# Kernel tuning notes

Measured on AMD Instinct MI355X. Metric: run time of the kernel, lower is better.

## Reference

```python
import jax, jax.numpy as jnp
import numpy as np
from jax import lax

K = 5
SCALE = 100.0
IN_CHN = 128
OUT_CHN = 128
KS = 3
STRIDE = 1
PAD = 1
N_W = OUT_CHN * IN_CHN * KS * KS


def setup_inputs() -> dict:
    key = jax.random.key(0)
    k1, k2, k3, k4, k5 = jax.random.split(key, 5)
    x = jax.random.normal(k1, (32, IN_CHN, 56, 56), dtype=jnp.float32)
    Alpha = jax.random.uniform(k2, (OUT_CHN, 1, 1), dtype=jnp.float32)
    # xavier-normal-ish init for M, Z
    M = jax.random.normal(k3, (OUT_CHN, IN_CHN, KS, KS), dtype=jnp.float32) * 0.05
    Z = jax.random.normal(k4, (K, OUT_CHN, IN_CHN, KS, KS), dtype=jnp.float32) * 0.05
    # rv ~ N(0, 1/sqrt(scale)) of shape (1, K); sample is all-zeros so the random branch is taken
    rv = jax.random.normal(k5, (1, K), dtype=jnp.float32) / np.float32(np.sqrt(SCALE))
    return {"x": x, "Alpha": Alpha, "M": M, "Z": Z, "rv": rv}


def reference(x, Alpha, M, Z, rv):
    # --- SDP weight synthesis (normalization is done under no_grad in torch) ---
    m = M.reshape(N_W)                # (N,)
    z = Z.reshape(K, N_W)             # (K, N)
    A = m * m + jnp.sum(z * z, axis=0) / SCALE
    inv = lax.rsqrt(A)
    m_n = m * inv
    z_n = z * inv
    w = (rv @ z_n + m_n).reshape(OUT_CHN, IN_CHN, KS, KS)  # (O,I,k,k)
    # --- sign binarization of weights and activations (ReCU) ---
    bw = jnp.sign(w)
    ba = jnp.sign(x)
    # --- conv2d, NCHW/OIHW ---
    out = lax.conv_general_dilated(
        ba, bw,
        window_strides=(STRIDE, STRIDE),
        padding=[(PAD, PAD), (PAD, PAD)],
        dimension_numbers=("NCHW", "OIHW", "NCHW"),
    )
    out = out * Alpha  # Alpha (O,1,1) broadcasts over (B,O,H,W)
    return out
```

## Files before the change

### kernel.cpp

```cpp
#include <hip/hip_runtime.h>
#include <stdint.h>

typedef unsigned int u32;
typedef unsigned long long u64;

#define HW      3136
#define PADW    58
#define PADHW   3364

#define WB_OFF   0
#define BF_OFF   18432
#define N2A_OFF  23040
#define AB_OFF   23552

#define NB_W     128
#define NB_A     392
#define NB_R     29

__global__ __launch_bounds__(256) void k_prep(
    const float* __restrict__ x, const float* __restrict__ Alpha,
    const float* __restrict__ M, const float* __restrict__ Z,
    const float* __restrict__ rv, char* __restrict__ ws)
{
  int t = threadIdx.x;
  if (blockIdx.x < NB_W) {
    u32*   wb  = (u32*)(ws + WB_OFF);
    float* Bf  = (float*)(ws + BF_OFF);
    float* n2a = (float*)(ws + N2A_OFF);
    __shared__ float sw[1152];
    __shared__ u32 sbits[36];
    __shared__ int spc[9];
    int o = blockIdx.x;
    float r0 = rv[0], r1 = rv[1], r2 = rv[2], r3 = rv[3], r4 = rv[4];
    const float4* M4 = (const float4*)M;
    const float4* Z4 = (const float4*)Z;
    float4* sw4 = (float4*)sw;

    for (int j = t; j < 288; j += 256) {
      float4 a = M4[o * 288 + j];
      float4 z;
      z = Z4[0 * 36864 + o * 288 + j];
      a.x = fmaf(r0, z.x, a.x); a.y = fmaf(r0, z.y, a.y);
      a.z = fmaf(r0, z.z, a.z); a.w = fmaf(r0, z.w, a.w);
      z = Z4[1 * 36864 + o * 288 + j];
      a.x = fmaf(r1, z.x, a.x); a.y = fmaf(r1, z.y, a.y);
      a.z = fmaf(r1, z.z, a.z); a.w = fmaf(r1, z.w, a.w);
      z = Z4[2 * 36864 + o * 288 + j];
      a.x = fmaf(r2, z.x, a.x); a.y = fmaf(r2, z.y, a.y);
      a.z = fmaf(r2, z.z, a.z); a.w = fmaf(r2, z.w, a.w);
      z = Z4[3 * 36864 + o * 288 + j];
      a.x = fmaf(r3, z.x, a.x); a.y = fmaf(r3, z.y, a.y);
      a.z = fmaf(r3, z.z, a.z); a.w = fmaf(r3, z.w, a.w);
      z = Z4[4 * 36864 + o * 288 + j];
      a.x = fmaf(r4, z.x, a.x); a.y = fmaf(r4, z.y, a.y);
      a.z = fmaf(r4, z.z, a.z); a.w = fmaf(r4, z.w, a.w);
      sw4[j] = a;
    }
    __syncthreads();

    if (t < 36) {
      int tap = t >> 2;
      int wd  = t & 3;
      u32 bits = 0;
#pragma unroll
      for (int c = 0; c < 32; ++c) {
        float v = sw[(wd * 32 + c) * 9 + tap];
        bits |= (v > 0.0f ? 1u : 0u) << c;
      }
      wb[(o * 9 + tap) * 4 + wd] = bits;
      sbits[t] = bits;
    }
    __syncthreads();
    if (t < 9)
      spc[t] = __popc(sbits[4 * t]) + __popc(sbits[4 * t + 1])
             + __popc(sbits[4 * t + 2]) + __popc(sbits[4 * t + 3]);
    __syncthreads();
    if (t < 9) {
      int ht = t / 3, wt = t - ht * 3;
      int corr = 0;
#pragma unroll
      for (int tap = 0; tap < 9; ++tap) {
        int dh = tap / 3, dw = tap - dh * 3;
        int inv = ((ht == 0) & (dh == 0)) | ((ht == 2) & (dh == 2)) |
                  ((wt == 0) & (dw == 0)) | ((wt == 2) & (dw == 2));
        if (inv) corr += 128 - 2 * spc[tap];
      }
      Bf[t * 128 + o] = (float)(1152 - corr) * Alpha[o];
    }
    if (t == 0) n2a[o] = -2.0f * Alpha[o];
  } else if (blockIdx.x < NB_W + NB_A) {
    u32* abw = (u32*)(ws + AB_OFF);
    int idx = (blockIdx.x - NB_W) * 256 + t;
    int bg  = idx / 784;
    int q   = idx - bg * 784;
    int b   = bg >> 2;
    int g   = bg & 3;
    int h   = q / 14;
    int w0  = (q - h * 14) * 4;

    const float4* X4 = (const float4*)x
        + ((size_t)b * 128 + g * 32) * (HW / 4) + q;
    u32 m0 = 0, m1 = 0, m2 = 0, m3 = 0;
#pragma unroll
    for (int c = 0; c < 32; ++c) {
      float4 f = X4[(size_t)c * (HW / 4)];
      m0 |= (f.x > 0.0f ? 1u : 0u) << c;
      m1 |= (f.y > 0.0f ? 1u : 0u) << c;
      m2 |= (f.z > 0.0f ? 1u : 0u) << c;
      m3 |= (f.w > 0.0f ? 1u : 0u) << c;
    }
    size_t base = ((size_t)b * PADHW + (h + 1) * PADW + (w0 + 1)) * 4 + g;
    abw[base]      = m0;
    abw[base + 4]  = m1;
    abw[base + 8]  = m2;
    abw[base + 12] = m3;
  } else {
    uint4* ab4 = (uint4*)(ws + AB_OFF);
    int e = (blockIdx.x - NB_W - NB_A) * 256 + t;
    if (e >= 32 * 228) return;
    int b  = e / 228;
    int r  = e - b * 228;
    int pp;
    if      (r < 58)  pp = r;
    else if (r < 116) pp = 57 * PADW + (r - 58);
    else {
      int s = r - 116;
      pp = (1 + (s >> 1)) * PADW + ((s & 1) ? 57 : 0);
    }
    ab4[(size_t)b * PADHW + pp] = make_uint4(0, 0, 0, 0);
  }
}

__global__ __launch_bounds__(64) void k_conv(
    const char* __restrict__ ws, float* __restrict__ out)
{
  const uint4*  ab  = (const uint4*)(ws + AB_OFF);
  const uint4*  wbg = (const uint4*)(ws + WB_OFF);
  const float*  BfG = (const float*)(ws + BF_OFF);
  const float*  n2a = (const float*)(ws + N2A_OFF);

  __shared__ uint4 swb[72];
  __shared__ float sBf[9][8];
  __shared__ float sn2a[8];
  int tid = threadIdx.x;
  int og  = blockIdx.y;
  int o0  = og * 8;
#pragma unroll
  for (int j = tid; j < 72; j += 64) {
    swb[j] = wbg[o0 * 9 + j];
    (&sBf[0][0])[j] = BfG[(j >> 3) * 128 + o0 + (j & 7)];
  }
  if (tid < 8) sn2a[tid] = n2a[o0 + tid];
  __syncthreads();

  int q  = blockIdx.x * 64 + tid;
  int b  = q / 784;
  int r  = q - b * 784;
  int h  = r / 14;
  int w4 = r - h * 14;
  int w0 = w4 * 4;

  const uint4* ap = ab + ((size_t)b * PADW + h) * PADW + w0;
  u32 A[3][6][4];
#pragma unroll
  for (int rr = 0; rr < 3; ++rr)
#pragma unroll
    for (int cc = 0; cc < 6; ++cc) {
      uint4 v = ap[(size_t)rr * PADW + cc];
      A[rr][cc][0] = v.x; A[rr][cc][1] = v.y;
      A[rr][cc][2] = v.z; A[rr][cc][3] = v.w;
    }

  int ht  = (h == 0) ? 0 : (h == 55 ? 6 : 3);
  int cl0 = ht + ((w0 == 0) ? 0 : 1);
  int cl1 = ht + 1;
  int cl3 = ht + ((w0 == 52) ? 2 : 1);

  float* outp = out + ((size_t)b * 128 + o0) * HW + h * 56 + w0;

#pragma unroll
  for (int oi = 0; oi < 8; ++oi) {
    int s0 = 0, s1 = 0, s2 = 0, s3 = 0;
#pragma unroll
    for (int dh = 0; dh < 3; ++dh)
#pragma unroll
      for (int dw = 0; dw < 3; ++dw) {
        uint4 wv = swb[oi * 9 + dh * 3 + dw];
#pragma unroll
        for (int k = 0; k < 4; ++k) {
          u32 wk = (&wv.x)[k];
          s0 += __popc(A[dh][dw + 0][k] ^ wk);
          s1 += __popc(A[dh][dw + 1][k] ^ wk);
          s2 += __popc(A[dh][dw + 2][k] ^ wk);
          s3 += __popc(A[dh][dw + 3][k] ^ wk);
        }
      }
    float na = sn2a[oi];
    float4 ov;
    ov.x = fmaf((float)s0, na, sBf[cl0][oi]);
    ov.y = fmaf((float)s1, na, sBf[cl1][oi]);
    ov.z = fmaf((float)s2, na, sBf[cl1][oi]);
    ov.w = fmaf((float)s3, na, sBf[cl3][oi]);
    *(float4*)(outp + (size_t)oi * HW) = ov;
  }
}

extern "C" void kernel_launch(void* const* d_in, const int* in_sizes, int n_in,
                              void* d_out, int out_size, void* d_ws, size_t ws_size,
                              hipStream_t stream)
{
  const float* x     = (const float*)d_in[0];
  const float* Alpha = (const float*)d_in[1];
  const float* M     = (const float*)d_in[2];
  const float* Z     = (const float*)d_in[3];
  const float* rv    = (const float*)d_in[4];
  float* out         = (float*)d_out;
  char*  ws          = (char*)d_ws;

  k_prep<<<NB_W + NB_A + NB_R, 256, 0, stream>>>(x, Alpha, M, Z, rv, ws);
  k_conv<<<dim3(392, 16), 64, 0, stream>>>(ws, out);
}
```

Baseline: 135.8 us.

## Fuse prep and conv into one cooperative kernel with grid sync

Merges the weight/activation binarization kernel and the XNOR-popcount conv kernel into a single cooperative launch of 784 blocks of 256 threads separated by a grid-wide sync. Each block now computes 16 output channels instead of 8. The aim is to remove the second kernel launch and its launch gap. In exchange, all blocks must be co-resident, the grid barrier itself costs time, and occupancy is constrained. The old two-kernel path stays as a fallback when cooperative launch is not possible.

```diff
diff --git a/kernel.cpp b/kernel.cpp
--- a/kernel.cpp
+++ b/kernel.cpp
@@ -1,5 +1,8 @@
 #include <hip/hip_runtime.h>
+#include <hip/hip_cooperative_groups.h>
 #include <stdint.h>
+
+namespace cg = cooperative_groups;
 
 typedef unsigned int u32;
 typedef unsigned long long u64;
@@ -17,20 +20,30 @@
 #define NB_A     392
 #define NB_R     29
 
-__global__ __launch_bounds__(256) void k_prep(
+#define QB_PER_OG 98
+#define FB_BLOCKS 784
+
+__global__ __launch_bounds__(256, 4) void k_fused(
     const float* __restrict__ x, const float* __restrict__ Alpha,
     const float* __restrict__ M, const float* __restrict__ Z,
-    const float* __restrict__ rv, char* __restrict__ ws)
+    const float* __restrict__ rv, char* __restrict__ ws,
+    float* __restrict__ out)
 {
-  int t = threadIdx.x;
-  if (blockIdx.x < NB_W) {
+  __shared__ float sw[1152];
+  __shared__ u32   sbits[36];
+  __shared__ int   spc[9];
+  __shared__ uint4 swb[144];
+  __shared__ float sBf[9][16];
+  __shared__ float sn2a[16];
+
+  int t   = threadIdx.x;
+  int blk = blockIdx.x;
+
+  if (blk < NB_W) {
     u32*   wb  = (u32*)(ws + WB_OFF);
     float* Bf  = (float*)(ws + BF_OFF);
     float* n2a = (float*)(ws + N2A_OFF);
-    __shared__ float sw[1152];
-    __shared__ u32 sbits[36];
-    __shared__ int spc[9];
-    int o = blockIdx.x;
+    int o = blk;
     float r0 = rv[0], r1 = rv[1], r2 = rv[2], r3 = rv[3], r4 = rv[4];
     const float4* M4 = (const float4*)M;
     const float4* Z4 = (const float4*)Z;
@@ -88,6 +101,190 @@
       Bf[t * 128 + o] = (float)(1152 - corr) * Alpha[o];
     }
     if (t == 0) n2a[o] = -2.0f * Alpha[o];
+  } else if (blk < NB_W + NB_A) {
+    u32* abw = (u32*)(ws + AB_OFF);
+    int idx = (blk - NB_W) * 256 + t;
+    int bg  = idx / 784;
+    int q   = idx - bg * 784;
+    int b   = bg >> 2;
+    int g   = bg & 3;
+    int h   = q / 14;
+    int w0  = (q - h * 14) * 4;
+
+    const float4* X4 = (const float4*)x
+        + ((size_t)b * 128 + g * 32) * (HW / 4) + q;
+    u32 m0 = 0, m1 = 0, m2 = 0, m3 = 0;
+#pragma unroll 8
+    for (int c = 0; c < 32; ++c) {
+      float4 f = X4[(size_t)c * (HW / 4)];
+      m0 |= (f.x > 0.0f ? 1u : 0u) << c;
+      m1 |= (f.y > 0.0f ? 1u : 0u) << c;
+      m2 |= (f.z > 0.0f ? 1u : 0u) << c;
+      m3 |= (f.w > 0.0f ? 1u : 0u) << c;
+    }
+    size_t base = ((size_t)b * PADHW + (h + 1) * PADW + (w0 + 1)) * 4 + g;
+    abw[base]      = m0;
+    abw[base + 4]  = m1;
+    abw[base + 8]  = m2;
+    abw[base + 12] = m3;
+  } else if (blk < NB_W + NB_A + NB_R) {
+    uint4* ab4 = (uint4*)(ws + AB_OFF);
+    int e = (blk - NB_W - NB_A) * 256 + t;
+    if (e < 32 * 228) {
+      int b  = e / 228;
+      int r  = e - b * 228;
+      int pp;
+      if      (r < 58)  pp = r;
+      else if (r < 116) pp = 57 * PADW + (r - 58);
+      else {
+        int s = r - 116;
+        pp = (1 + (s >> 1)) * PADW + ((s & 1) ? 57 : 0);
+      }
+      ab4[(size_t)b * PADHW + pp] = make_uint4(0, 0, 0, 0);
+    }
+  }
+
+  cg::this_grid().sync();
+
+  const uint4* ab   = (const uint4*)(ws + AB_OFF);
+  const uint4* wbg  = (const uint4*)(ws + WB_OFF);
+  const float* BfG  = (const float*)(ws + BF_OFF);
+  const float* n2aG = (const float*)(ws + N2A_OFF);
+
+  int ogpair = blk / QB_PER_OG;
+  int qblk   = blk - ogpair * QB_PER_OG;
+  int o0     = ogpair * 16;
+
+  if (t < 144) {
+    swb[t] = wbg[o0 * 9 + t];
+    (&sBf[0][0])[t] = BfG[(t >> 4) * 128 + o0 + (t & 15)];
+  }
+  if (t < 16) sn2a[t] = n2aG[o0 + t];
+  __syncthreads();
+
+  int q  = qblk * 256 + t;
+  int b  = q / 784;
+  int r  = q - b * 784;
+  int h  = r / 14;
+  int w4 = r - h * 14;
+  int w0 = w4 * 4;
+
+  const uint4* ap = ab + (size_t)b * PADHW + (size_t)h * PADW + w0;
+  u32 A[3][6][4];
+#pragma unroll
+  for (int rr = 0; rr < 3; ++rr)
+#pragma unroll
+    for (int cc = 0; cc < 6; ++cc) {
+      uint4 v = ap[(size_t)rr * PADW + cc];
+      A[rr][cc][0] = v.x; A[rr][cc][1] = v.y;
+      A[rr][cc][2] = v.z; A[rr][cc][3] = v.w;
+    }
+
+  int ht  = (h == 0) ? 0 : (h == 55 ? 6 : 3);
+  int cl0 = ht + ((w0 == 0) ? 0 : 1);
+  int cl1 = ht + 1;
+  int cl3 = ht + ((w0 == 52) ? 2 : 1);
+
+  float* outp = out + ((size_t)b * 128 + o0) * HW + h * 56 + w0;
+
+#pragma unroll 2
+  for (int oi = 0; oi < 16; ++oi) {
+    int s0 = 0, s1 = 0, s2 = 0, s3 = 0;
+#pragma unroll
+    for (int dh = 0; dh < 3; ++dh)
+#pragma unroll
+      for (int dw = 0; dw < 3; ++dw) {
+        uint4 wv = swb[oi * 9 + dh * 3 + dw];
+#pragma unroll
+        for (int k = 0; k < 4; ++k) {
+          u32 wk = (&wv.x)[k];
+          s0 += __popc(A[dh][dw + 0][k] ^ wk);
+          s1 += __popc(A[dh][dw + 1][k] ^ wk);
+          s2 += __popc(A[dh][dw + 2][k] ^ wk);
+          s3 += __popc(A[dh][dw + 3][k] ^ wk);
+        }
+      }
+    float na = sn2a[oi];
+    float4 ov;
+    ov.x = fmaf((float)s0, na, sBf[cl0][oi]);
+    ov.y = fmaf((float)s1, na, sBf[cl1][oi]);
+    ov.z = fmaf((float)s2, na, sBf[cl1][oi]);
+    ov.w = fmaf((float)s3, na, sBf[cl3][oi]);
+    *(float4*)(outp + (size_t)oi * HW) = ov;
+  }
+}
+
+__global__ __launch_bounds__(256) void k_prep(
+    const float* __restrict__ x, const float* __restrict__ Alpha,
+    const float* __restrict__ M, const float* __restrict__ Z,
+    const float* __restrict__ rv, char* __restrict__ ws)
+{
+  int t = threadIdx.x;
+  if (blockIdx.x < NB_W) {
+    u32*   wb  = (u32*)(ws + WB_OFF);
+    float* Bf  = (float*)(ws + BF_OFF);
+    float* n2a = (float*)(ws + N2A_OFF);
+    __shared__ float sw[1152];
+    __shared__ u32 sbits[36];
+    __shared__ int spc[9];
+    int o = blockIdx.x;
+    float r0 = rv[0], r1 = rv[1], r2 = rv[2], r3 = rv[3], r4 = rv[4];
+    const float4* M4 = (const float4*)M;
+    const float4* Z4 = (const float4*)Z;
+    float4* sw4 = (float4*)sw;
+
+    for (int j = t; j < 288; j += 256) {
+      float4 a = M4[o * 288 + j];
+      float4 z;
+      z = Z4[0 * 36864 + o * 288 + j];
+      a.x = fmaf(r0, z.x, a.x); a.y = fmaf(r0, z.y, a.y);
+      a.z = fmaf(r0, z.z, a.z); a.w = fmaf(r0, z.w, a.w);
+      z = Z4[1 * 36864 + o * 288 + j];
+      a.x = fmaf(r1, z.x, a.x); a.y = fmaf(r1, z.y, a.y);
+      a.z = fmaf(r1, z.z, a.z); a.w = fmaf(r1, z.w, a.w);
+      z = Z4[2 * 36864 + o * 288 + j];
+      a.x = fmaf(r2, z.x, a.x); a.y = fmaf(r2, z.y, a.y);
+      a.z = fmaf(r2, z.z, a.z); a.w = fmaf(r2, z.w, a.w);
+      z = Z4[3 * 36864 + o * 288 + j];
+      a.x = fmaf(r3, z.x, a.x); a.y = fmaf(r3, z.y, a.y);
+      a.z = fmaf(r3, z.z, a.z); a.w = fmaf(r3, z.w, a.w);
+      z = Z4[4 * 36864 + o * 288 + j];
+      a.x = fmaf(r4, z.x, a.x); a.y = fmaf(r4, z.y, a.y);
+      a.z = fmaf(r4, z.z, a.z); a.w = fmaf(r4, z.w, a.w);
+      sw4[j] = a;
+    }
+    __syncthreads();
+
+    if (t < 36) {
+      int tap = t >> 2;
+      int wd  = t & 3;
+      u32 bits = 0;
+#pragma unroll
+      for (int c = 0; c < 32; ++c) {
+        float v = sw[(wd * 32 + c) * 9 + tap];
+        bits |= (v > 0.0f ? 1u : 0u) << c;
+      }
+      wb[(o * 9 + tap) * 4 + wd] = bits;
+      sbits[t] = bits;
+    }
+    __syncthreads();
+    if (t < 9)
+      spc[t] = __popc(sbits[4 * t]) + __popc(sbits[4 * t + 1])
+             + __popc(sbits[4 * t + 2]) + __popc(sbits[4 * t + 3]);
+    __syncthreads();
+    if (t < 9) {
+      int ht = t / 3, wt = t - ht * 3;
+      int corr = 0;
+#pragma unroll
+      for (int tap = 0; tap < 9; ++tap) {
+        int dh = tap / 3, dw = tap - dh * 3;
+        int inv = ((ht == 0) & (dh == 0)) | ((ht == 2) & (dh == 2)) |
+                  ((wt == 0) & (dw == 0)) | ((wt == 2) & (dw == 2));
+        if (inv) corr += 128 - 2 * spc[tap];
+      }
+      Bf[t * 128 + o] = (float)(1152 - corr) * Alpha[o];
+    }
+    if (t == 0) n2a[o] = -2.0f * Alpha[o];
   } else if (blockIdx.x < NB_W + NB_A) {
     u32* abw = (u32*)(ws + AB_OFF);
     int idx = (blockIdx.x - NB_W) * 256 + t;
@@ -217,6 +414,26 @@
   float* out         = (float*)d_out;
   char*  ws          = (char*)d_ws;
 
+  static int coop_ok = -1;
+  if (coop_ok < 0) {
+    int nb = 0, ncu = 0;
+    hipError_t e1 = hipOccupancyMaxActiveBlocksPerMultiprocessor(
+        &nb, (const void*)k_fused, 256, 0);
+    hipError_t e2 = hipDeviceGetAttribute(
+        &ncu, hipDeviceAttributeMultiprocessorCount, 0);
+    coop_ok = (e1 == hipSuccess && e2 == hipSuccess &&
+               (long)nb * ncu >= FB_BLOCKS) ? 1 : 0;
+  }
+
+  if (coop_ok) {
+    void* args[] = {(void*)&x, (void*)&Alpha, (void*)&M, (void*)&Z,
+                    (void*)&rv, (void*)&ws, (void*)&out};
+    hipError_t err = hipLaunchCooperativeKernel(
+        (const void*)k_fused, dim3(FB_BLOCKS), dim3(256), args, 0, stream);
+    if (err == hipSuccess) return;
+    coop_ok = 0;
+  }
+
   k_prep<<<NB_W + NB_A + NB_R, 256, 0, stream>>>(x, Alpha, M, Z, rv, ws);
   k_conv<<<dim3(392, 16), 64, 0, stream>>>(ws, out);
 }
```

Measured after the change: 133.9 us. No clear change (-1.4%).

## Fuse activation binarization into conv kernel with LDS-staged row bands

Applied to the files above, without the earlier changes.

Activation sign-packing moves out of the prep kernel and into the conv kernel. Each block binarizes a 4-row band (plus halo) of one image into shared memory, zero-padded there, and computes all 128 output channels from it. The padded bit-packed activation buffer in the workspace and its border-zeroing pass are removed, saving a global round trip. The cost is 448 large blocks that each re-read the halo rows, load the full weight bits into LDS, and carry a heavier per-thread loop, which may lower occupancy and parallelism.

```diff
diff --git a/kernel.cpp b/kernel.cpp
--- a/kernel.cpp
+++ b/kernel.cpp
@@ -5,203 +5,196 @@
 typedef unsigned long long u64;
 
 #define HW      3136
-#define PADW    58
-#define PADHW   3364
 
 #define WB_OFF   0
 #define BF_OFF   18432
 #define N2A_OFF  23040
-#define AB_OFF   23552
-
-#define NB_W     128
-#define NB_A     392
-#define NB_R     29
-
-__global__ __launch_bounds__(256) void k_prep(
-    const float* __restrict__ x, const float* __restrict__ Alpha,
-    const float* __restrict__ M, const float* __restrict__ Z,
-    const float* __restrict__ rv, char* __restrict__ ws)
+
+__global__ __launch_bounds__(256) void k_wsyn(
+    const float* __restrict__ Alpha, const float* __restrict__ M,
+    const float* __restrict__ Z, const float* __restrict__ rv,
+    char* __restrict__ ws)
 {
   int t = threadIdx.x;
-  if (blockIdx.x < NB_W) {
-    u32*   wb  = (u32*)(ws + WB_OFF);
-    float* Bf  = (float*)(ws + BF_OFF);
-    float* n2a = (float*)(ws + N2A_OFF);
-    __shared__ float sw[1152];
-    __shared__ u32 sbits[36];
-    __shared__ int spc[9];
-    int o = blockIdx.x;
-    float r0 = rv[0], r1 = rv[1], r2 = rv[2], r3 = rv[3], r4 = rv[4];
-    const float4* M4 = (const float4*)M;
-    const float4* Z4 = (const float4*)Z;
-    float4* sw4 = (float4*)sw;
-
-    for (int j = t; j < 288; j += 256) {
-      float4 a = M4[o * 288 + j];
-      float4 z;
-      z = Z4[0 * 36864 + o * 288 + j];
-      a.x = fmaf(r0, z.x, a.x); a.y = fmaf(r0, z.y, a.y);
-      a.z = fmaf(r0, z.z, a.z); a.w = fmaf(r0, z.w, a.w);
-      z = Z4[1 * 36864 + o * 288 + j];
-      a.x = fmaf(r1, z.x, a.x); a.y = fmaf(r1, z.y, a.y);
-      a.z = fmaf(r1, z.z, a.z); a.w = fmaf(r1, z.w, a.w);
-      z = Z4[2 * 36864 + o * 288 + j];
-      a.x = fmaf(r2, z.x, a.x); a.y = fmaf(r2, z.y, a.y);
-      a.z = fmaf(r2, z.z, a.z); a.w = fmaf(r2, z.w, a.w);
-      z = Z4[3 * 36864 + o * 288 + j];
-      a.x = fmaf(r3, z.x, a.x); a.y = fmaf(r3, z.y, a.y);
-      a.z = fmaf(r3, z.z, a.z); a.w = fmaf(r3, z.w, a.w);
-      z = Z4[4 * 36864 + o * 288 + j];
-      a.x = fmaf(r4, z.x, a.x); a.y = fmaf(r4, z.y, a.y);
-      a.z = fmaf(r4, z.z, a.z); a.w = fmaf(r4, z.w, a.w);
-      sw4[j] = a;
-    }
-    __syncthreads();
-
-    if (t < 36) {
-      int tap = t >> 2;
-      int wd  = t & 3;
-      u32 bits = 0;
-#pragma unroll
+  u32*   wb  = (u32*)(ws + WB_OFF);
+  float* Bf  = (float*)(ws + BF_OFF);
+  float* n2a = (float*)(ws + N2A_OFF);
+  __shared__ float sw[1152];
+  __shared__ u32 sbits[36];
+  __shared__ int spc[9];
+  int o = blockIdx.x;
+  float r0 = rv[0], r1 = rv[1], r2 = rv[2], r3 = rv[3], r4 = rv[4];
+  const float4* M4 = (const float4*)M;
+  const float4* Z4 = (const float4*)Z;
+  float4* sw4 = (float4*)sw;
+
+  for (int j = t; j < 288; j += 256) {
+    float4 a = M4[o * 288 + j];
+    float4 z;
+    z = Z4[0 * 36864 + o * 288 + j];
+    a.x = fmaf(r0, z.x, a.x); a.y = fmaf(r0, z.y, a.y);
+    a.z = fmaf(r0, z.z, a.z); a.w = fmaf(r0, z.w, a.w);
+    z = Z4[1 * 36864 + o * 288 + j];
+    a.x = fmaf(r1, z.x, a.x); a.y = fmaf(r1, z.y, a.y);
+    a.z = fmaf(r1, z.z, a.z); a.w = fmaf(r1, z.w, a.w);
+    z = Z4[2 * 36864 + o * 288 + j];
+    a.x = fmaf(r2, z.x, a.x); a.y = fmaf(r2, z.y, a.y);
+    a.z = fmaf(r2, z.z, a.z); a.w = fmaf(r2, z.w, a.w);
+    z = Z4[3 * 36864 + o * 288 + j];
+    a.x = fmaf(r3, z.x, a.x); a.y = fmaf(r3, z.y, a.y);
+    a.z = fmaf(r3, z.z, a.z); a.w = fmaf(r3, z.w, a.w);
+    z = Z4[4 * 36864 + o * 288 + j];
+    a.x = fmaf(r4, z.x, a.x); a.y = fmaf(r4, z.y, a.y);
+    a.z = fmaf(r4, z.z, a.z); a.w = fmaf(r4, z.w, a.w);
+    sw4[j] = a;
+  }
+  __syncthreads();
+
+  if (t < 36) {
+    int tap = t >> 2;
+    int wd  = t & 3;
+    u32 bits = 0;
+#pragma unroll
+    for (int c = 0; c < 32; ++c) {
+      float v = sw[(wd * 32 + c) * 9 + tap];
+      bits |= (v > 0.0f ? 1u : 0u) << c;
+    }
+    wb[(o * 9 + tap) * 4 + wd] = bits;
+    sbits[t] = bits;
+  }
+  __syncthreads();
+  if (t < 9)
+    spc[t] = __popc(sbits[4 * t]) + __popc(sbits[4 * t + 1])
+           + __popc(sbits[4 * t + 2]) + __popc(sbits[4 * t + 3]);
+  __syncthreads();
+  if (t < 9) {
+    int ht = t / 3, wt = t - ht * 3;
+    int corr = 0;
+#pragma unroll
+    for (int tap = 0; tap < 9; ++tap) {
+      int dh = tap / 3, dw = tap - dh * 3;
+      int inv = ((ht == 0) & (dh == 0)) | ((ht == 2) & (dh == 2)) |
+                ((wt == 0) & (dw == 0)) | ((wt == 2) & (dw == 2));
+      if (inv) corr += 128 - 2 * spc[tap];
+    }
+    Bf[t * 128 + o] = (float)(1152 - corr) * Alpha[o];
+  }
+  if (t == 0) n2a[o] = -2.0f * Alpha[o];
+}
+
+__global__ __launch_bounds__(256) void k_conv2(
+    const float* __restrict__ x, const char* __restrict__ ws,
+    float* __restrict__ out)
+{
+  __shared__ uint4 sab[6 * 58];
+  __shared__ uint4 swb[1160];
+  __shared__ float sBfX[9 * 136];
+  __shared__ float sn2aX[136];
+
+  const uint4* wbg  = (const uint4*)(ws + WB_OFF);
+  const float* BfG  = (const float*)(ws + BF_OFF);
+  const float* n2aG = (const float*)(ws + N2A_OFF);
+
+  int t    = threadIdx.x;
+  int blk  = blockIdx.x;
+  int b    = blk / 14;
+  int band = blk - b * 14;
+  int h0   = band * 4;
+
+  for (int j = t; j < 1152; j += 256) {
+    int o = j / 9, tap = j - o * 9;
+    swb[o * 9 + (o >> 4) + tap] = wbg[j];
+    int cl = j >> 7, oo = j & 127;
+    sBfX[cl * 136 + oo + (oo >> 4)] = BfG[j];
+  }
+  if (t < 128) sn2aX[t + (t >> 4)] = n2aG[t];
+  {
+    u32* sz = (u32*)sab;
+    for (int j = t; j < 6 * 58 * 4; j += 256) sz[j] = 0;
+  }
+  __syncthreads();
+
+  u32* sabw = (u32*)sab;
+  for (int i = t; i < 336; i += 256) {
+    int g    = i & 3;
+    int rq   = i >> 2;
+    int row  = rq / 14;
+    int quad = rq - row * 14;
+    int in_row = h0 - 1 + row;
+    if (in_row >= 0 && in_row < 56) {
+      const float4* X4 = (const float4*)x
+          + ((size_t)(b * 128 + g * 32)) * (HW / 4) + in_row * 14 + quad;
+      u32 m0 = 0, m1 = 0, m2 = 0, m3 = 0;
+#pragma unroll 8
       for (int c = 0; c < 32; ++c) {
-        float v = sw[(wd * 32 + c) * 9 + tap];
-        bits |= (v > 0.0f ? 1u : 0u) << c;
+        float4 f = X4[(size_t)c * (HW / 4)];
+        m0 |= (f.x > 0.0f ? 1u : 0u) << c;
+        m1 |= (f.y > 0.0f ? 1u : 0u) << c;
+        m2 |= (f.z > 0.0f ? 1u : 0u) << c;
+        m3 |= (f.w > 0.0f ? 1u : 0u) << c;
       }
-      wb[(o * 9 + tap) * 4 + wd] = bits;
-      sbits[t] = bits;
-    }
-    __syncthreads();
-    if (t < 9)
-      spc[t] = __popc(sbits[4 * t]) + __popc(sbits[4 * t + 1])
-             + __popc(sbits[4 * t + 2]) + __popc(sbits[4 * t + 3]);
-    __syncthreads();
-    if (t < 9) {
-      int ht = t / 3, wt = t - ht * 3;
-      int corr = 0;
-#pragma unroll
-      for (int tap = 0; tap < 9; ++tap) {
-        int dh = tap / 3, dw = tap - dh * 3;
-        int inv = ((ht == 0) & (dh == 0)) | ((ht == 2) & (dh == 2)) |
-                  ((wt == 0) & (dw == 0)) | ((wt == 2) & (dw == 2));
-        if (inv) corr += 128 - 2 * spc[tap];
+      int colb = (row * 58 + 1 + quad * 4) * 4 + g;
+      sabw[colb]      = m0;
+      sabw[colb + 4]  = m1;
+      sabw[colb + 8]  = m2;
+      sabw[colb + 12] = m3;
+    }
+  }
+  __syncthreads();
+
+  for (int task = t; task < 448; task += 256) {
+    int og = task & 7;
+    int qd = task >> 3;
+    int r  = qd / 14;
+    int w4 = qd - r * 14;
+    int w0 = w4 * 4;
+    int h  = h0 + r;
+    int o0 = og * 16;
+
+    u32 A[3][6][4];
+#pragma unroll
+    for (int rr = 0; rr < 3; ++rr)
+#pragma unroll
+      for (int cc = 0; cc < 6; ++cc) {
+        uint4 v = sab[(r + rr) * 58 + w0 + cc];
+        A[rr][cc][0] = v.x; A[rr][cc][1] = v.y;
+        A[rr][cc][2] = v.z; A[rr][cc][3] = v.w;
       }
-      Bf[t * 128 + o] = (float)(1152 - corr) * Alpha[o];
-    }
-    if (t == 0) n2a[o] = -2.0f * Alpha[o];
-  } else if (blockIdx.x < NB_W + NB_A) {
-    u32* abw = (u32*)(ws + AB_OFF);
-    int idx = (blockIdx.x - NB_W) * 256 + t;
-    int bg  = idx / 784;
-    int q   = idx - bg * 784;
-    int b   = bg >> 2;
-    int g   = bg & 3;
-    int h   = q / 14;
-    int w0  = (q - h * 14) * 4;
-
-    const float4* X4 = (const float4*)x
-        + ((size_t)b * 128 + g * 32) * (HW / 4) + q;
-    u32 m0 = 0, m1 = 0, m2 = 0, m3 = 0;
-#pragma unroll
-    for (int c = 0; c < 32; ++c) {
-      float4 f = X4[(size_t)c * (HW / 4)];
-      m0 |= (f.x > 0.0f ? 1u : 0u) << c;
-      m1 |= (f.y > 0.0f ? 1u : 0u) << c;
-      m2 |= (f.z > 0.0f ? 1u : 0u) << c;
-      m3 |= (f.w > 0.0f ? 1u : 0u) << c;
-    }
-    size_t base = ((size_t)b * PADHW + (h + 1) * PADW + (w0 + 1)) * 4 + g;
-    abw[base]      = m0;
-    abw[base + 4]  = m1;
-    abw[base + 8]  = m2;
-    abw[base + 12] = m3;
-  } else {
-    uint4* ab4 = (uint4*)(ws + AB_OFF);
-    int e = (blockIdx.x - NB_W - NB_A) * 256 + t;
-    if (e >= 32 * 228) return;
-    int b  = e / 228;
-    int r  = e - b * 228;
-    int pp;
-    if      (r < 58)  pp = r;
-    else if (r < 116) pp = 57 * PADW + (r - 58);
-    else {
-      int s = r - 116;
-      pp = (1 + (s >> 1)) * PADW + ((s & 1) ? 57 : 0);
-    }
-    ab4[(size_t)b * PADHW + pp] = make_uint4(0, 0, 0, 0);
-  }
-}
-
-__global__ __launch_bounds__(64) void k_conv(
-    const char* __restrict__ ws, float* __restrict__ out)
-{
-  const uint4*  ab  = (const uint4*)(ws + AB_OFF);
-  const uint4*  wbg = (const uint4*)(ws + WB_OFF);
-  const float*  BfG = (const float*)(ws + BF_OFF);
-  const float*  n2a = (const float*)(ws + N2A_OFF);
-
-  __shared__ uint4 swb[72];
-  __shared__ float sBf[9][8];
-  __shared__ float sn2a[8];
-  int tid = threadIdx.x;
-  int og  = blockIdx.y;
-  int o0  = og * 8;
-#pragma unroll
-  for (int j = tid; j < 72; j += 64) {
-    swb[j] = wbg[o0 * 9 + j];
-    (&sBf[0][0])[j] = BfG[(j >> 3) * 128 + o0 + (j & 7)];
-  }
-  if (tid < 8) sn2a[tid] = n2a[o0 + tid];
-  __syncthreads();
-
-  int q  = blockIdx.x * 64 + tid;
-  int b  = q / 784;
-  int r  = q - b * 784;
-  int h  = r / 14;
-  int w4 = r - h * 14;
-  int w0 = w4 * 4;
-
-  const uint4* ap = ab + ((size_t)b * PADW + h) * PADW + w0;
-  u32 A[3][6][4];
-#pragma unroll
-  for (int rr = 0; rr < 3; ++rr)
-#pragma unroll
-    for (int cc = 0; cc < 6; ++cc) {
-      uint4 v = ap[(size_t)rr * PADW + cc];
-      A[rr][cc][0] = v.x; A[rr][cc][1] = v.y;
-      A[rr][cc][2] = v.z; A[rr][cc][3] = v.w;
-    }
-
-  int ht  = (h == 0) ? 0 : (h == 55 ? 6 : 3);
-  int cl0 = ht + ((w0 == 0) ? 0 : 1);
-  int cl1 = ht + 1;
-  int cl3 = ht + ((w0 == 52) ? 2 : 1);
-
-  float* outp = out + ((size_t)b * 128 + o0) * HW + h * 56 + w0;
-
-#pragma unroll
-  for (int oi = 0; oi < 8; ++oi) {
-    int s0 = 0, s1 = 0, s2 = 0, s3 = 0;
-#pragma unroll
-    for (int dh = 0; dh < 3; ++dh)
-#pragma unroll
-      for (int dw = 0; dw < 3; ++dw) {
-        uint4 wv = swb[oi * 9 + dh * 3 + dw];
-#pragma unroll
-        for (int k = 0; k < 4; ++k) {
-          u32 wk = (&wv.x)[k];
-          s0 += __popc(A[dh][dw + 0][k] ^ wk);
-          s1 += __popc(A[dh][dw + 1][k] ^ wk);
-          s2 += __popc(A[dh][dw + 2][k] ^ wk);
-          s3 += __popc(A[dh][dw + 3][k] ^ wk);
+
+    int ht  = (h == 0) ? 0 : (h == 55 ? 6 : 3);
+    int cl0 = ht + ((w0 == 0) ? 0 : 1);
+    int cl1 = ht + 1;
+    int cl3 = ht + ((w0 == 52) ? 2 : 1);
+
+    const uint4* wp   = &swb[o0 * 9 + og];
+    int          oX   = o0 + og;
+    float*       outp = out + ((size_t)(b * 128 + o0)) * HW + h * 56 + w0;
+
+#pragma unroll 4
+    for (int oi = 0; oi < 16; ++oi) {
+      int s0 = 0, s1 = 0, s2 = 0, s3 = 0;
+#pragma unroll
+      for (int dh = 0; dh < 3; ++dh)
+#pragma unroll
+        for (int dw = 0; dw < 3; ++dw) {
+          uint4 wv = wp[oi * 9 + dh * 3 + dw];
+#pragma unroll
+          for (int k = 0; k < 4; ++k) {
+            u32 wk = (&wv.x)[k];
+            s0 += __popc(A[dh][dw + 0][k] ^ wk);
+            s1 += __popc(A[dh][dw + 1][k] ^ wk);
+            s2 += __popc(A[dh][dw + 2][k] ^ wk);
+            s3 += __popc(A[dh][dw + 3][k] ^ wk);
+          }
         }
-      }
-    float na = sn2a[oi];
-    float4 ov;
-    ov.x = fmaf((float)s0, na, sBf[cl0][oi]);
-    ov.y = fmaf((float)s1, na, sBf[cl1][oi]);
-    ov.z = fmaf((float)s2, na, sBf[cl1][oi]);
-    ov.w = fmaf((float)s3, na, sBf[cl3][oi]);
-    *(float4*)(outp + (size_t)oi * HW) = ov;
+      float na = sn2aX[oX + oi];
+      float4 ov;
+      ov.x = fmaf((float)s0, na, sBfX[cl0 * 136 + oX + oi]);
+      ov.y = fmaf((float)s1, na, sBfX[cl1 * 136 + oX + oi]);
+      ov.z = fmaf((float)s2, na, sBfX[cl1 * 136 + oX + oi]);
+      ov.w = fmaf((float)s3, na, sBfX[cl3 * 136 + oX + oi]);
+      *(float4*)(outp + (size_t)oi * HW) = ov;
+    }
   }
 }
 
@@ -217,6 +210,6 @@
   float* out         = (float*)d_out;
   char*  ws          = (char*)d_ws;
 
-  k_prep<<<NB_W + NB_A + NB_R, 256, 0, stream>>>(x, Alpha, M, Z, rv, ws);
-  k_conv<<<dim3(392, 16), 64, 0, stream>>>(ws, out);
+  k_wsyn<<<128, 256, 0, stream>>>(Alpha, M, Z, rv, ws);
+  k_conv2<<<448, 256, 0, stream>>>(x, ws, out);
 }
```

After: 149.7 us. +10.3%, slower.
